# Optimization experiments

Measured on AMD Instinct MI355X. Metric: run time of the kernel, lower is better.

## Reference

```python
import jax, jax.numpy as jnp
import numpy as np

TINY = 1e-8
B, T, D = 128, 32, 400


def _offsets(T):
    offs, off = [], 0
    for lvl in range(T):
        offs.append(off)
        off += T - lvl
    return offs


def _inside_indices(T):
    # For level l, span start i (L = T - l spans), split k in [0, l):
    #   left child  = cell(offs[k] + i)             (span (i, level k))
    #   right child = cell(offs[l-k-1] + i + k + 1) (span (i+k+1, level l-k-1))
    offs = _offsets(T)
    out = {}
    for level in range(1, T):
        L = T - level
        lidx = np.empty((L, level), np.int32)
        ridx = np.empty((L, level), np.int32)
        for i in range(L):
            for k in range(level):
                lidx[i, k] = offs[k] + i
                ridx[i, k] = offs[level - k - 1] + i + k + 1
        out[level] = (jnp.asarray(lidx.reshape(-1)), jnp.asarray(ridx.reshape(-1)))
    return offs, out


def unit_norm(x):
    n = jnp.sqrt(jnp.sum(x * x, axis=-1, keepdims=True))
    return x / jnp.maximum(n, TINY)


def setup_inputs() -> dict:
    key = jax.random.key(0)
    ks = jax.random.split(key, 12)
    sc = 1.0 / np.sqrt(D).astype(np.float32)
    return {
        'x': jax.random.normal(ks[0], (B, T, D), jnp.float32),
        'w_leaf_h': jax.random.normal(ks[1], (D, D), jnp.float32) * sc,
        'b_leaf_h': jax.random.normal(ks[2], (D,), jnp.float32) * sc,
        'w_leaf_c': jax.random.normal(ks[3], (D, D), jnp.float32) * sc,
        'b_leaf_c': jax.random.normal(ks[4], (D,), jnp.float32) * sc,
        'u_lh': jax.random.normal(ks[5], (D, D), jnp.float32) * sc,
        'u_rh': jax.random.normal(ks[6], (D, D), jnp.float32) * sc,
        'b_h': jax.random.normal(ks[7], (D,), jnp.float32) * sc,
        'u_lc': jax.random.normal(ks[8], (D, D), jnp.float32) * sc,
        'u_rc': jax.random.normal(ks[9], (D, D), jnp.float32) * sc,
        'b_c': jax.random.normal(ks[10], (D,), jnp.float32) * sc,
        'w_score': jax.random.normal(ks[11], (D, D), jnp.float32) * sc,
    }


def reference(x, w_leaf_h, b_leaf_h, w_leaf_c, b_leaf_c,
              u_lh, u_rh, b_h, u_lc, u_rc, b_c, w_score):
    Bb, Tt, Dd = x.shape
    offs, idx = _inside_indices(Tt)
    ncells = Tt * (Tt + 1) // 2
    # leaf_transform + unit normalize
    h0 = unit_norm(jnp.tanh(x @ w_leaf_h + b_leaf_h))
    c0 = unit_norm(jnp.tanh(x @ w_leaf_c + b_leaf_c))
    ch = jnp.zeros((Bb, ncells, Dd), x.dtype).at[:, :Tt].set(h0)
    cc = jnp.zeros((Bb, ncells, Dd), x.dtype).at[:, :Tt].set(c0)
    cs = jnp.zeros((Bb, ncells, 1), x.dtype)
    for level in range(1, Tt):  # fixed structural loop over tree levels
        L, N = Tt - level, level
        lidx, ridx = idx[level]
        lh, rh = ch[:, lidx], ch[:, ridx]  # gather: [B, L*N, D]
        lc, rc = cc[:, lidx], cc[:, ridx]
        ls, rs = cs[:, lidx], cs[:, ridx]  # [B, L*N, 1]
        # compose
        h = jnp.tanh(lh @ u_lh + rh @ u_rh + b_h)
        c = jnp.tanh(lc @ u_lc + rc @ u_rc + b_c)
        # bilinear score + child scores, softmax over splits N
        s = jnp.einsum('bnd,de,bne->bn', lh, w_score, rh)[..., None] + ls + rs
        s = s.reshape(Bb, L, N, 1)
        p = jax.nn.softmax(s, axis=2)
        h_agg = unit_norm(jnp.sum(h.reshape(Bb, L, N, Dd) * p, axis=2))
        c_agg = unit_norm(jnp.sum(c.reshape(Bb, L, N, Dd) * p, axis=2))
        s_agg = jnp.sum(s * p, axis=2)
        off = offs[level]
        ch = ch.at[:, off:off + L].set(h_agg)
        cc = cc.at[:, off:off + L].set(c_agg)
        cs = cs.at[:, off:off + L].set(s_agg)
    return ch
```

## Files before the change

kernel.cpp:

```cpp
#include <hip/hip_runtime.h>
#include <hip/hip_bf16.h>
#include <stdint.h>


#define BB 128
#define TT 32
#define DD 400
#define NCELLS 528
#define NW 2000
#define KP 416

typedef __attribute__((ext_vector_type(8))) short s8v;
typedef __attribute__((ext_vector_type(4))) float f32x4;

__device__ __forceinline__ int offs_of(int v) { return v * TT - (v * (v - 1)) / 2; }

__device__ __forceinline__ float asf(uint32_t bits) {
    union { uint32_t i; float f; } v; v.i = bits; return v.f;
}
__device__ __forceinline__ uint16_t f2bf(float f) {
    union { float f; uint32_t i; } v; v.f = f;
    uint32_t x = v.i;
    return (uint16_t)((x + 0x7fffu + ((x >> 16) & 1u)) >> 16);
}
__device__ __forceinline__ float tanh_fast(float x) {
    float e = __builtin_amdgcn_exp2f(x * 2.8853900817779268f);
    return 1.f - 2.f * __builtin_amdgcn_rcpf(e + 1.f);
}

__device__ __forceinline__ void block_reduce2(float& a, float& b, float* sred) {
#pragma unroll
    for (int o = 32; o > 0; o >>= 1) { a += __shfl_down(a, o); b += __shfl_down(b, o); }
    int lane = threadIdx.x & 63, w = threadIdx.x >> 6;
    if (lane == 0) { sred[w] = a; sred[4 + w] = b; }
    __syncthreads();
    a = sred[0] + sred[1] + sred[2] + sred[3];
    b = sred[4] + sred[5] + sred[6] + sred[7];
    __syncthreads();
}

__global__ void pack_k(const float* __restrict__ u_lh, const float* __restrict__ u_rh,
                       const float* __restrict__ w_score, const float* __restrict__ u_lc,
                       const float* __restrict__ u_rc, const float* __restrict__ w_leaf_h,
                       const float* __restrict__ w_leaf_c, const float* __restrict__ x,
                       uint16_t* __restrict__ WT, uint16_t* __restrict__ WLT,
                       uint16_t* __restrict__ XB) {
    int idx = blockIdx.x * blockDim.x + threadIdx.x;
    const int nWT = NW * KP, nWLT = 800 * KP, nXB = 4096 * KP;
    if (idx < nWT) {
        int n = idx / KP, k = idx - n * KP;
        float v = 0.f;
        if (k < DD) {
            const float* src = (n < 400) ? u_lh : (n < 800) ? u_rh : (n < 1200) ? w_score
                               : (n < 1600) ? u_lc : u_rc;
            v = src[k * DD + (n % 400)];
        }
        WT[idx] = f2bf(v);
    } else if (idx < nWT + nWLT) {
        int q = idx - nWT; int n = q / KP, k = q - n * KP;
        float v = 0.f;
        if (k < DD) v = (n < 400) ? w_leaf_h[k * DD + n] : w_leaf_c[k * DD + (n - 400)];
        WLT[q] = f2bf(v);
    } else if (idx < nWT + nWLT + nXB) {
        int q = idx - nWT - nWLT; int r = q / KP, k = q - r * KP;
        XB[q] = f2bf(k < DD ? x[(size_t)r * DD + k] : 0.f);
    }
}

__global__ __launch_bounds__(256)
void tgemm_k(const uint16_t* __restrict__ XB, const uint16_t* __restrict__ WLT,
             float* __restrict__ PREout) {
    __shared__ short As[256][40];
    __shared__ short Ws[80][40];
    const int t = threadIdx.x, lane = t & 63, w = t >> 6;
    const int n0 = blockIdx.x * 80;
    const int tile_m = blockIdx.y * 256;

    const int arow_l = t >> 2, asub = t & 3;
    const uint16_t* aptr[4];
#pragma unroll
    for (int p = 0; p < 4; p++) {
        int gr = tile_m + arow_l + 64 * p;
        aptr[p] = XB + (size_t)gr * KP + asub * 8;
    }
    const uint16_t* wptr0 = WLT + (size_t)(n0 + (t >> 2)) * KP + (t & 3) * 8;
    const uint16_t* wptr1 = WLT + (size_t)(n0 + 64 + (t >> 2)) * KP + (t & 3) * 8;

    const int frow = lane & 15, kcol = (lane >> 4) * 8;
    f32x4 acc[4][5];
#pragma unroll
    for (int mi = 0; mi < 4; mi++)
#pragma unroll
        for (int ni = 0; ni < 5; ni++) acc[mi][ni] = (f32x4)(0.f);

    for (int k0 = 0; k0 < KP; k0 += 32) {
        s8v av[4];
#pragma unroll
        for (int p = 0; p < 4; p++) av[p] = *(const s8v*)(aptr[p] + k0);
        s8v wv0 = *(const s8v*)(wptr0 + k0);
        s8v wv1;
        if (t < 64) wv1 = *(const s8v*)(wptr1 + k0);
        __syncthreads();
#pragma unroll
        for (int p = 0; p < 4; p++) *(s8v*)&As[arow_l + 64 * p][asub * 8] = av[p];
        *(s8v*)&Ws[t >> 2][(t & 3) * 8] = wv0;
        if (t < 64) *(s8v*)&Ws[64 + (t >> 2)][(t & 3) * 8] = wv1;
        __syncthreads();
        s8v a[4];
#pragma unroll
        for (int mi = 0; mi < 4; mi++)
            a[mi] = *(const s8v*)&As[64 * w + 16 * mi + frow][kcol];
#pragma unroll
        for (int ni = 0; ni < 5; ni++) {
            s8v bv = *(const s8v*)&Ws[16 * ni + frow][kcol];
#pragma unroll
            for (int mi = 0; mi < 4; mi++)
                acc[mi][ni] = __builtin_amdgcn_mfma_f32_16x16x32_bf16(a[mi], bv, acc[mi][ni], 0, 0, 0);
        }
    }
#pragma unroll
    for (int mi = 0; mi < 4; mi++) {
        int rbase = tile_m + 64 * w + 16 * mi + 4 * (lane >> 4);
#pragma unroll
        for (int i = 0; i < 4; i++) {
            int gr = rbase + i;
            float* o = PREout + (size_t)gr * 800 + n0 + frow;
#pragma unroll
            for (int ni = 0; ni < 5; ni++) o[16 * ni] = acc[mi][ni][i];
        }
    }
}

__global__ __launch_bounds__(256)
void tpgemm_k(const uint16_t* __restrict__ HB, const uint16_t* __restrict__ CB,
              const uint16_t* __restrict__ WT,
              uint16_t* __restrict__ LP, uint16_t* __restrict__ RP,
              uint16_t* __restrict__ G, int Lcur, int cellbase) {
    __shared__ short AsH[128][40];
    __shared__ short AsC[128][40];
    __shared__ short WsH[80][40];
    __shared__ short WsC[80][40];
    const int t = threadIdx.x, lane = t & 63, w = t >> 6;
    const int nch = blockIdx.x % 5, kind = blockIdx.x / 5;
    const int n0 = nch * 80;
    const int tile_m = blockIdx.y * 128;
    const bool doC = (kind != 2);

    const int wh0 = (kind == 0) ? n0 : (kind == 1) ? 400 + n0 : 800 + n0;
    const int wc0 = (kind == 0) ? 1200 + n0 : 1600 + n0;

    const int arow_l = t >> 2, asub = t & 3;
    const uint16_t *aptrH[2], *aptrC[2];
#pragma unroll
    for (int p = 0; p < 2; p++) {
        int gr = tile_m + arow_l + 64 * p;
        int rb = gr / Lcur, ri = gr - rb * Lcur;
        aptrH[p] = HB + (size_t)(rb * NCELLS + cellbase + ri) * DD + asub * 8;
        aptrC[p] = CB + (size_t)(rb * 32 + ri) * DD + asub * 8;
    }
    const uint16_t* wptrH0 = WT + (size_t)(wh0 + (t >> 2)) * KP + (t & 3) * 8;
    const uint16_t* wptrH1 = WT + (size_t)(wh0 + 64 + (t >> 2)) * KP + (t & 3) * 8;
    const uint16_t* wptrC0 = WT + (size_t)(wc0 + (t >> 2)) * KP + (t & 3) * 8;
    const uint16_t* wptrC1 = WT + (size_t)(wc0 + 64 + (t >> 2)) * KP + (t & 3) * 8;

    const int frow = lane & 15, kcol = (lane >> 4) * 8;
    f32x4 accH[2][5], accC[2][5];
#pragma unroll
    for (int mi = 0; mi < 2; mi++)
#pragma unroll
        for (int ni = 0; ni < 5; ni++) { accH[mi][ni] = (f32x4)(0.f); accC[mi][ni] = (f32x4)(0.f); }

    for (int k0 = 0; k0 < KP; k0 += 32) {
        s8v avH0 = *(const s8v*)(aptrH[0] + k0);
        s8v avH1 = *(const s8v*)(aptrH[1] + k0);
        s8v wvH0 = *(const s8v*)(wptrH0 + k0);
        s8v wvH1;
        if (t < 64) wvH1 = *(const s8v*)(wptrH1 + k0);
        s8v avC0, avC1, wvC0, wvC1;
        if (doC) {
            avC0 = *(const s8v*)(aptrC[0] + k0);
            avC1 = *(const s8v*)(aptrC[1] + k0);
            wvC0 = *(const s8v*)(wptrC0 + k0);
            if (t < 64) wvC1 = *(const s8v*)(wptrC1 + k0);
        }
        __syncthreads();
        *(s8v*)&AsH[arow_l][asub * 8] = avH0;
        *(s8v*)&AsH[arow_l + 64][asub * 8] = avH1;
        *(s8v*)&WsH[t >> 2][(t & 3) * 8] = wvH0;
        if (t < 64) *(s8v*)&WsH[64 + (t >> 2)][(t & 3) * 8] = wvH1;
        if (doC) {
            *(s8v*)&AsC[arow_l][asub * 8] = avC0;
            *(s8v*)&AsC[arow_l + 64][asub * 8] = avC1;
            *(s8v*)&WsC[t >> 2][(t & 3) * 8] = wvC0;
            if (t < 64) *(s8v*)&WsC[64 + (t >> 2)][(t & 3) * 8] = wvC1;
        }
        __syncthreads();
        s8v aH0 = *(const s8v*)&AsH[32 * w + frow][kcol];
        s8v aH1 = *(const s8v*)&AsH[32 * w + 16 + frow][kcol];
        s8v aC0, aC1;
        if (doC) {
            aC0 = *(const s8v*)&AsC[32 * w + frow][kcol];
            aC1 = *(const s8v*)&AsC[32 * w + 16 + frow][kcol];
        }
#pragma unroll
        for (int ni = 0; ni < 5; ni++) {
            s8v bvH = *(const s8v*)&WsH[16 * ni + frow][kcol];
            accH[0][ni] = __builtin_amdgcn_mfma_f32_16x16x32_bf16(aH0, bvH, accH[0][ni], 0, 0, 0);
            accH[1][ni] = __builtin_amdgcn_mfma_f32_16x16x32_bf16(aH1, bvH, accH[1][ni], 0, 0, 0);
            if (doC) {
                s8v bvC = *(const s8v*)&WsC[16 * ni + frow][kcol];
                accC[0][ni] = __builtin_amdgcn_mfma_f32_16x16x32_bf16(aC0, bvC, accC[0][ni], 0, 0, 0);
                accC[1][ni] = __builtin_amdgcn_mfma_f32_16x16x32_bf16(aC1, bvC, accC[1][ni], 0, 0, 0);
            }
        }
    }

    if (kind == 2) {
#pragma unroll
        for (int mi = 0; mi < 2; mi++) {
            int rbase = tile_m + 32 * w + 16 * mi + 4 * (lane >> 4);
#pragma unroll
            for (int i = 0; i < 4; i++) {
                int gr = rbase + i;
                int rb = gr / Lcur, ri = gr - rb * Lcur;
                size_t row = (size_t)(rb * NCELLS + cellbase + ri);
                uint16_t* o = G + row * 400 + n0 + frow;
#pragma unroll
                for (int ni = 0; ni < 5; ni++) o[16 * ni] = f2bf(accH[mi][ni][i]);
            }
        }
    } else {
        uint16_t* tb = (kind == 0) ? LP : RP;
#pragma unroll
        for (int mi = 0; mi < 2; mi++) {
            int rbase = tile_m + 32 * w + 16 * mi + 4 * (lane >> 4);
#pragma unroll
            for (int i = 0; i < 4; i++) {
                int gr = rbase + i;
                int rb = gr / Lcur, ri = gr - rb * Lcur;
                size_t row = (size_t)(rb * NCELLS + cellbase + ri);
                uint32_t* o = (uint32_t*)(tb + row * 800) + n0 + frow;
#pragma unroll
                for (int ni = 0; ni < 5; ni++)
                    o[16 * ni] = (uint32_t)f2bf(accH[mi][ni][i])
                               | ((uint32_t)f2bf(accC[mi][ni][i]) << 16);
            }
        }
    }
}

__global__ __launch_bounds__(256)
void leaf_norm_k(const float* __restrict__ PRE, const float* __restrict__ blh,
                 const float* __restrict__ blc, float* __restrict__ Hchart,
                 uint16_t* __restrict__ HB, uint16_t* __restrict__ CB,
                 float* __restrict__ cs) {
    const int r = blockIdx.x;
    const int b = r >> 5, tt = r & 31;
    const int t = threadIdx.x;
    const int d = t * 2;
    float th0 = 0, th1 = 0, tc0 = 0, tc1 = 0;
    if (d < DD) {
        const float* p = PRE + (size_t)r * 800;
        th0 = tanh_fast(p[d] + blh[d]);
        th1 = tanh_fast(p[d + 1] + blh[d + 1]);
        tc0 = tanh_fast(p[400 + d] + blc[d]);
        tc1 = tanh_fast(p[400 + d + 1] + blc[d + 1]);
    }
    __shared__ float sred[8];
    float nh = th0 * th0 + th1 * th1, nc = tc0 * tc0 + tc1 * tc1;
    block_reduce2(nh, nc, sred);
    float rh = 1.f / fmaxf(sqrtf(nh), 1e-8f);
    float rc = 1.f / fmaxf(sqrtf(nc), 1e-8f);
    if (d < DD) {
        size_t ho = (size_t)(b * NCELLS + tt) * DD + d;
        float h0 = th0 * rh, h1 = th1 * rh, c0 = tc0 * rc, c1 = tc1 * rc;
        Hchart[ho] = h0; Hchart[ho + 1] = h1;
        *(uint32_t*)(HB + ho) = (uint32_t)f2bf(h0) | ((uint32_t)f2bf(h1) << 16);
        *(uint32_t*)(CB + (size_t)(b * 32 + tt) * DD + d) =
            (uint32_t)f2bf(c0) | ((uint32_t)f2bf(c1) << 16);
    }
    if (t == 0) cs[b * NCELLS + tt] = 0.f;
}

__global__ __launch_bounds__(256)
void level_k(float* __restrict__ Hchart, uint16_t* __restrict__ HB,
             uint16_t* __restrict__ CB, float* __restrict__ cs,
             const uint16_t* __restrict__ LP, const uint16_t* __restrict__ RP,
             const uint16_t* __restrict__ G,
             const float* __restrict__ b_h, const float* __restrict__ b_c, int level) {
    const int L = TT - level, N = level;
    const int blk = (blockIdx.x & 7) * (gridDim.x >> 3) + (blockIdx.x >> 3);
    const int b = blk / L, i = blk - b * L;
    const int cell = offs_of(level) + i;
    const int t = threadIdx.x, lane = t & 63, w = t >> 6;
    __shared__ float sh_s[32], sh_p[32];
    __shared__ float sred[8];

    for (int k = w; k < N; k += 4) {
        int lcell = offs_of(k) + i;
        int rcell = offs_of(level - k - 1) + i + k + 1;
        const uint32_t* g = (const uint32_t*)(G + (size_t)(b * NCELLS + lcell) * DD);
        const uint32_t* hr = (const uint32_t*)(HB + (size_t)(b * NCELLS + rcell) * DD);
        float s = 0.f;
        for (int d2 = lane; d2 < 200; d2 += 64) {
            uint32_t gv = g[d2], hv = hr[d2];
            s += asf(gv << 16) * asf(hv << 16)
               + asf(gv & 0xffff0000u) * asf(hv & 0xffff0000u);
        }
#pragma unroll
        for (int o = 32; o > 0; o >>= 1) s += __shfl_down(s, o);
        if (lane == 0) sh_s[k] = s + cs[b * NCELLS + lcell] + cs[b * NCELLS + rcell];
    }
    __syncthreads();

    if (t == 0) {
        float m = -1e30f;
        for (int k = 0; k < N; k++) m = fmaxf(m, sh_s[k]);
        float sum = 0.f;
        for (int k = 0; k < N; k++) {
            float e = __builtin_amdgcn_exp2f((sh_s[k] - m) * 1.4426950408889634f);
            sh_p[k] = e; sum += e;
        }
        float inv = 1.f / sum, sagg = 0.f;
        for (int k = 0; k < N; k++) { sh_p[k] *= inv; sagg += sh_p[k] * sh_s[k]; }
        cs[b * NCELLS + cell] = sagg;
    }
    __syncthreads();

    float ha0 = 0, ha1 = 0, ca0 = 0, ca1 = 0;
    const int d = t * 2;
    if (d < DD) {
        const float bh0 = b_h[d], bh1 = b_h[d + 1], bc0 = b_c[d], bc1 = b_c[d + 1];
        const uint16_t* lpb = LP + (size_t)(b * NCELLS) * 800 + 2 * d;
        const uint16_t* rpb = RP + (size_t)(b * NCELLS) * 800 + 2 * d;
        int lcell = i;
        int rcell = offs_of(level - 1) + i + 1;
        uint2 lv = *(const uint2*)(lpb + (size_t)lcell * 800);
        uint2 rv = *(const uint2*)(rpb + (size_t)rcell * 800);
        for (int k = 0; k < N; k++) {
            uint2 lc = lv, rc = rv;
            if (k + 1 < N) {
                int ln = offs_of(k + 1) + i;
                int rn = offs_of(level - k - 2) + i + k + 2;
                lv = *(const uint2*)(lpb + (size_t)ln * 800);
                rv = *(const uint2*)(rpb + (size_t)rn * 800);
            }
            float p = sh_p[k];
            ha0 += p * tanh_fast(asf(lc.x << 16) + asf(rc.x << 16) + bh0);
            ca0 += p * tanh_fast(asf(lc.x & 0xffff0000u) + asf(rc.x & 0xffff0000u) + bc0);
            ha1 += p * tanh_fast(asf(lc.y << 16) + asf(rc.y << 16) + bh1);
            ca1 += p * tanh_fast(asf(lc.y & 0xffff0000u) + asf(rc.y & 0xffff0000u) + bc1);
        }
    }
    float nh = ha0 * ha0 + ha1 * ha1, nc = ca0 * ca0 + ca1 * ca1;
    block_reduce2(nh, nc, sred);
    float rh = 1.f / fmaxf(sqrtf(nh), 1e-8f);
    float rc = 1.f / fmaxf(sqrtf(nc), 1e-8f);
    if (d < DD) {
        float h0 = ha0 * rh, h1 = ha1 * rh, c0 = ca0 * rc, c1 = ca1 * rc;
        size_t ho = (size_t)(b * NCELLS + cell) * DD + d;
        Hchart[ho] = h0; Hchart[ho + 1] = h1;
        *(uint32_t*)(HB + ho) = (uint32_t)f2bf(h0) | ((uint32_t)f2bf(h1) << 16);
        *(uint32_t*)(CB + (size_t)(b * 32 + i) * DD + d) =
            (uint32_t)f2bf(c0) | ((uint32_t)f2bf(c1) << 16);
    }
}

extern "C" void kernel_launch(void* const* d_in, const int* in_sizes, int n_in,
                              void* d_out, int out_size, void* d_ws, size_t ws_size,
                              hipStream_t stream) {
    const float* x        = (const float*)d_in[0];
    const float* w_leaf_h = (const float*)d_in[1];
    const float* b_leaf_h = (const float*)d_in[2];
    const float* w_leaf_c = (const float*)d_in[3];
    const float* b_leaf_c = (const float*)d_in[4];
    const float* u_lh     = (const float*)d_in[5];
    const float* u_rh     = (const float*)d_in[6];
    const float* b_h      = (const float*)d_in[7];
    const float* u_lc     = (const float*)d_in[8];
    const float* u_rc     = (const float*)d_in[9];
    const float* b_c      = (const float*)d_in[10];
    const float* w_score  = (const float*)d_in[11];
    float* Hchart = (float*)d_out;

    const size_t PL = (size_t)BB * NCELLS * DD;
    char* p = (char*)d_ws;
    uint16_t* LP = (uint16_t*)p; p += 2 * PL * sizeof(uint16_t);
    uint16_t* RP = (uint16_t*)p; p += 2 * PL * sizeof(uint16_t);
    uint16_t* G  = (uint16_t*)p; p += PL * sizeof(uint16_t);
    uint16_t* HB = (uint16_t*)p; p += PL * sizeof(uint16_t) + 64;
    uint16_t* CB = (uint16_t*)p; p += (size_t)BB * 32 * DD * sizeof(uint16_t) + 64;
    float* CS    = (float*)p;    p += (size_t)BB * NCELLS * sizeof(float);
    uint16_t* WT = (uint16_t*)p; p += (size_t)NW * KP * sizeof(uint16_t);
    float* PRE    = (float*)LP;
    uint16_t* WLT = RP;
    uint16_t* XB  = RP + (size_t)800 * KP;

    {
        int total = NW * KP + 800 * KP + 4096 * KP;
        pack_k<<<(total + 255) / 256, 256, 0, stream>>>(u_lh, u_rh, w_score, u_lc, u_rc,
                                                        w_leaf_h, w_leaf_c, x, WT, WLT, XB);
    }
    tgemm_k<<<dim3(10, 16), 256, 0, stream>>>(XB, WLT, PRE);
    leaf_norm_k<<<BB * TT, 256, 0, stream>>>(PRE, b_leaf_h, b_leaf_c, Hchart, HB, CB, CS);
    tpgemm_k<<<dim3(15, 32), 256, 0, stream>>>(HB, CB, WT, LP, RP, G, 32, 0);

    int off = TT;
    for (int level = 1; level < TT; ++level) {
        int L = TT - level;
        level_k<<<BB * L, 256, 0, stream>>>(Hchart, HB, CB, CS, LP, RP, G, b_h, b_c, level);
        if (level < TT - 1) {
            tpgemm_k<<<dim3(15, L), 256, 0, stream>>>(HB, CB, WT, LP, RP, G, L, off);
        }
        off += L;
    }
}
```

Baseline: 1.651 ms.

## Replace per-level kernel launches with persistent cooperative kernel using group barriers

Moves the 61 alternating level and projection-GEMM launches into one cooperative persistent kernel of 512 blocks. The blocks are split into 8 independent groups of 16 batch elements, and each group syncs through its own atomic-counter barrier between phases. This removes launch overhead and the device-wide drain between levels. In exchange, the tile count per group per level is small, which can leave blocks idle, and the spin barriers add latency. The old multi-launch path is kept as a fallback when occupancy is too low or the cooperative launch fails.

Measured after the change: 1.664 ms. Within noise of the previous version (+0.8%).

```diff
diff --git a/kernel.cpp b/kernel.cpp
--- a/kernel.cpp
+++ b/kernel.cpp
@@ -39,12 +39,22 @@
     __syncthreads();
 }
 
+__device__ __forceinline__ void group_barrier(uint32_t* cnt) {
+    __syncthreads();
+    if (threadIdx.x == 0) {
+        __hip_atomic_fetch_add(cnt, 1u, __ATOMIC_RELEASE, __HIP_MEMORY_SCOPE_AGENT);
+        while (__hip_atomic_load(cnt, __ATOMIC_ACQUIRE, __HIP_MEMORY_SCOPE_AGENT) < 64u)
+            __builtin_amdgcn_s_sleep(2);
+    }
+    __syncthreads();
+}
+
 __global__ void pack_k(const float* __restrict__ u_lh, const float* __restrict__ u_rh,
                        const float* __restrict__ w_score, const float* __restrict__ u_lc,
                        const float* __restrict__ u_rc, const float* __restrict__ w_leaf_h,
                        const float* __restrict__ w_leaf_c, const float* __restrict__ x,
                        uint16_t* __restrict__ WT, uint16_t* __restrict__ WLT,
-                       uint16_t* __restrict__ XB) {
+                       uint16_t* __restrict__ XB, uint32_t* __restrict__ CNT) {
     int idx = blockIdx.x * blockDim.x + threadIdx.x;
     const int nWT = NW * KP, nWLT = 800 * KP, nXB = 4096 * KP;
     if (idx < nWT) {
@@ -64,6 +74,8 @@
     } else if (idx < nWT + nWLT + nXB) {
         int q = idx - nWT - nWLT; int r = q / KP, k = q - r * KP;
         XB[q] = f2bf(k < DD ? x[(size_t)r * DD + k] : 0.f);
+    } else if (idx < nWT + nWLT + nXB + 512) {
+        CNT[idx - nWT - nWLT - nXB] = 0u;
     }
 }
 
@@ -131,19 +143,17 @@
     }
 }
 
-__global__ __launch_bounds__(256)
-void tpgemm_k(const uint16_t* __restrict__ HB, const uint16_t* __restrict__ CB,
-              const uint16_t* __restrict__ WT,
-              uint16_t* __restrict__ LP, uint16_t* __restrict__ RP,
-              uint16_t* __restrict__ G, int Lcur, int cellbase) {
-    __shared__ short AsH[128][40];
-    __shared__ short AsC[128][40];
-    __shared__ short WsH[80][40];
-    __shared__ short WsC[80][40];
+__device__ __forceinline__
+void tpgemm_tile(const uint16_t* __restrict__ HB, const uint16_t* __restrict__ CB,
+                 const uint16_t* __restrict__ WT,
+                 uint16_t* __restrict__ LP, uint16_t* __restrict__ RP,
+                 uint16_t* __restrict__ G,
+                 int Lq, int cellbase, int b_base, int nch, int kind,
+                 int tile_m, int Mtot,
+                 short (*AsH)[40], short (*AsC)[40],
+                 short (*WsH)[40], short (*WsC)[40]) {
     const int t = threadIdx.x, lane = t & 63, w = t >> 6;
-    const int nch = blockIdx.x % 5, kind = blockIdx.x / 5;
     const int n0 = nch * 80;
-    const int tile_m = blockIdx.y * 128;
     const bool doC = (kind != 2);
 
     const int wh0 = (kind == 0) ? n0 : (kind == 1) ? 400 + n0 : 800 + n0;
@@ -154,9 +164,10 @@
 #pragma unroll
     for (int p = 0; p < 2; p++) {
         int gr = tile_m + arow_l + 64 * p;
-        int rb = gr / Lcur, ri = gr - rb * Lcur;
-        aptrH[p] = HB + (size_t)(rb * NCELLS + cellbase + ri) * DD + asub * 8;
-        aptrC[p] = CB + (size_t)(rb * 32 + ri) * DD + asub * 8;
+        if (gr >= Mtot) gr = 0;
+        int rb = gr / Lq, ri = gr - rb * Lq;
+        aptrH[p] = HB + (size_t)((b_base + rb) * NCELLS + cellbase + ri) * DD + asub * 8;
+        aptrC[p] = CB + (size_t)((b_base + rb) * 32 + ri) * DD + asub * 8;
     }
     const uint16_t* wptrH0 = WT + (size_t)(wh0 + (t >> 2)) * KP + (t & 3) * 8;
     const uint16_t* wptrH1 = WT + (size_t)(wh0 + 64 + (t >> 2)) * KP + (t & 3) * 8;
@@ -222,8 +233,9 @@
 #pragma unroll
             for (int i = 0; i < 4; i++) {
                 int gr = rbase + i;
-                int rb = gr / Lcur, ri = gr - rb * Lcur;
-                size_t row = (size_t)(rb * NCELLS + cellbase + ri);
+                if (gr >= Mtot) continue;
+                int rb = gr / Lq, ri = gr - rb * Lq;
+                size_t row = (size_t)((b_base + rb) * NCELLS + cellbase + ri);
                 uint16_t* o = G + row * 400 + n0 + frow;
 #pragma unroll
                 for (int ni = 0; ni < 5; ni++) o[16 * ni] = f2bf(accH[mi][ni][i]);
@@ -237,8 +249,9 @@
 #pragma unroll
             for (int i = 0; i < 4; i++) {
                 int gr = rbase + i;
-                int rb = gr / Lcur, ri = gr - rb * Lcur;
-                size_t row = (size_t)(rb * NCELLS + cellbase + ri);
+                if (gr >= Mtot) continue;
+                int rb = gr / Lq, ri = gr - rb * Lq;
+                size_t row = (size_t)((b_base + rb) * NCELLS + cellbase + ri);
                 uint32_t* o = (uint32_t*)(tb + row * 800) + n0 + frow;
 #pragma unroll
                 for (int ni = 0; ni < 5; ni++)
@@ -247,6 +260,17 @@
             }
         }
     }
+}
+
+__global__ __launch_bounds__(256)
+void tpgemm_k(const uint16_t* __restrict__ HB, const uint16_t* __restrict__ CB,
+              const uint16_t* __restrict__ WT,
+              uint16_t* __restrict__ LP, uint16_t* __restrict__ RP,
+              uint16_t* __restrict__ G, int Lcur, int cellbase) {
+    __shared__ short AsH[128][40], AsC[128][40], WsH[80][40], WsC[80][40];
+    tpgemm_tile(HB, CB, WT, LP, RP, G, Lcur, cellbase, 0,
+                blockIdx.x % 5, blockIdx.x / 5, blockIdx.y * 128, 128 * Lcur,
+                AsH, AsC, WsH, WsC);
 }
 
 __global__ __launch_bounds__(256)
@@ -282,19 +306,17 @@
     if (t == 0) cs[b * NCELLS + tt] = 0.f;
 }
 
-__global__ __launch_bounds__(256)
-void level_k(float* __restrict__ Hchart, uint16_t* __restrict__ HB,
-             uint16_t* __restrict__ CB, float* __restrict__ cs,
-             const uint16_t* __restrict__ LP, const uint16_t* __restrict__ RP,
-             const uint16_t* __restrict__ G,
-             const float* __restrict__ b_h, const float* __restrict__ b_c, int level) {
-    const int L = TT - level, N = level;
-    const int blk = (blockIdx.x & 7) * (gridDim.x >> 3) + (blockIdx.x >> 3);
-    const int b = blk / L, i = blk - b * L;
+__device__ void level_cell(float* __restrict__ Hchart, uint16_t* __restrict__ HB,
+                           uint16_t* __restrict__ CB, float* __restrict__ cs,
+                           const uint16_t* __restrict__ LP, const uint16_t* __restrict__ RP,
+                           const uint16_t* __restrict__ G,
+                           const float* __restrict__ b_h, const float* __restrict__ b_c,
+                           int level, int b, int i,
+                           float* sh_s, float* sh_p, float* sred) {
+    const int N = level;
     const int cell = offs_of(level) + i;
     const int t = threadIdx.x, lane = t & 63, w = t >> 6;
-    __shared__ float sh_s[32], sh_p[32];
-    __shared__ float sred[8];
+    __syncthreads();
 
     for (int k = w; k < N; k += 4) {
         int lcell = offs_of(k) + i;
@@ -366,6 +388,60 @@
     }
 }
 
+__global__ __launch_bounds__(256)
+void level_k(float* __restrict__ Hchart, uint16_t* __restrict__ HB,
+             uint16_t* __restrict__ CB, float* __restrict__ cs,
+             const uint16_t* __restrict__ LP, const uint16_t* __restrict__ RP,
+             const uint16_t* __restrict__ G,
+             const float* __restrict__ b_h, const float* __restrict__ b_c, int level) {
+    __shared__ float sh_s[32], sh_p[32], sred[8];
+    const int L = TT - level;
+    const int blk = (blockIdx.x & 7) * (gridDim.x >> 3) + (blockIdx.x >> 3);
+    level_cell(Hchart, HB, CB, cs, LP, RP, G, b_h, b_c, level,
+               blk / L, blk % L, sh_s, sh_p, sred);
+}
+
+struct GArgs {
+    float* Hchart; uint16_t* HB; uint16_t* CB; float* CS;
+    uint16_t* LP; uint16_t* RP; uint16_t* G; const uint16_t* WT;
+    const float* b_h; const float* b_c; uint32_t* CNT;
+};
+
+__global__ __launch_bounds__(256)
+void diora_groups_k(GArgs A) {
+    __shared__ short AsH[128][40], AsC[128][40], WsH[80][40], WsC[80][40];
+    __shared__ float sh_s[32], sh_p[32], sred[8];
+    const int g = blockIdx.x & 7;
+    const int jj = blockIdx.x >> 3;
+    const int b_base = g * 16;
+    uint32_t* cnt = A.CNT + g * 62;
+    int seq = 0;
+
+    int off = TT;
+    for (int lv = 1; lv < TT; ++lv) {
+        const int L = TT - lv;
+        for (int ci = jj; ci < 16 * L; ci += 64) {
+            int bl = ci / L, i = ci - bl * L;
+            level_cell(A.Hchart, A.HB, A.CB, A.CS, A.LP, A.RP, A.G,
+                       A.b_h, A.b_c, lv, b_base + bl, i, sh_s, sh_p, sred);
+        }
+        if (lv < TT - 1) {
+            group_barrier(cnt + seq); seq++;
+            const int Mtot = 16 * L;
+            const int Mt = (Mtot + 127) >> 7;
+            const int ntiles = 15 * Mt;
+            for (int tile = jj; tile < ntiles; tile += 64) {
+                int tx = tile % 15, ty = tile / 15;
+                tpgemm_tile(A.HB, A.CB, A.WT, A.LP, A.RP, A.G,
+                            L, off, b_base, tx % 5, tx / 5, ty * 128, Mtot,
+                            AsH, AsC, WsH, WsC);
+            }
+            group_barrier(cnt + seq); seq++;
+        }
+        off += L;
+    }
+}
+
 extern "C" void kernel_launch(void* const* d_in, const int* in_sizes, int n_in,
                               void* d_out, int out_size, void* d_ws, size_t ws_size,
                               hipStream_t stream) {
@@ -392,26 +468,41 @@
     uint16_t* CB = (uint16_t*)p; p += (size_t)BB * 32 * DD * sizeof(uint16_t) + 64;
     float* CS    = (float*)p;    p += (size_t)BB * NCELLS * sizeof(float);
     uint16_t* WT = (uint16_t*)p; p += (size_t)NW * KP * sizeof(uint16_t);
+    uint32_t* CNT= (uint32_t*)p; p += 512 * sizeof(uint32_t);
     float* PRE    = (float*)LP;
     uint16_t* WLT = RP;
     uint16_t* XB  = RP + (size_t)800 * KP;
 
     {
-        int total = NW * KP + 800 * KP + 4096 * KP;
+        int total = NW * KP + 800 * KP + 4096 * KP + 512;
         pack_k<<<(total + 255) / 256, 256, 0, stream>>>(u_lh, u_rh, w_score, u_lc, u_rc,
-                                                        w_leaf_h, w_leaf_c, x, WT, WLT, XB);
+                                                        w_leaf_h, w_leaf_c, x, WT, WLT, XB, CNT);
     }
     tgemm_k<<<dim3(10, 16), 256, 0, stream>>>(XB, WLT, PRE);
     leaf_norm_k<<<BB * TT, 256, 0, stream>>>(PRE, b_leaf_h, b_leaf_c, Hchart, HB, CB, CS);
     tpgemm_k<<<dim3(15, 32), 256, 0, stream>>>(HB, CB, WT, LP, RP, G, 32, 0);
 
-    int off = TT;
-    for (int level = 1; level < TT; ++level) {
-        int L = TT - level;
-        level_k<<<BB * L, 256, 0, stream>>>(Hchart, HB, CB, CS, LP, RP, G, b_h, b_c, level);
-        if (level < TT - 1) {
-            tpgemm_k<<<dim3(15, L), 256, 0, stream>>>(HB, CB, WT, LP, RP, G, L, off);
-        }
-        off += L;
-    }
-}
+    int occ = 0;
+    hipError_t qerr = hipOccupancyMaxActiveBlocksPerMultiprocessor(
+        &occ, (const void*)diora_groups_k, 256, 0);
+    bool coop_ok = (qerr == hipSuccess) && (occ * 256 >= 512);
+    if (coop_ok) {
+        GArgs ga{Hchart, HB, CB, CS, LP, RP, G, WT, b_h, b_c, CNT};
+        void* kargs[] = {&ga};
+        hipError_t lerr = hipLaunchCooperativeKernel((void*)diora_groups_k, dim3(512),
+                                                     dim3(256), kargs, 0, stream);
+        if (lerr != hipSuccess) coop_ok = false;
+    }
+    if (!coop_ok) {
+        int off = TT;
+        for (int level = 1; level < TT; ++level) {
+            int L = TT - level;
+            level_k<<<BB * L, 256, 0, stream>>>(Hchart, HB, CB, CS, LP, RP, G,
+                                                b_h, b_c, level);
+            if (level < TT - 1) {
+                tpgemm_k<<<dim3(15, L), 256, 0, stream>>>(HB, CB, WT, LP, RP, G, L, off);
+            }
+            off += L;
+        }
+    }
+}
```
